# Performance work log

Measured on AMD Instinct MI355X. Metric: run time of the kernel, lower is better.

The kernel has to match this reference:

```python
import jax, jax.numpy as jnp
import numpy as np

B, N, C = 8, 4096, 512

def setup_inputs() -> dict:
    key = jax.random.key(0)
    ks = jax.random.split(key, 6)
    s = 1.0 / np.sqrt(C)
    return {
        "x": jax.random.normal(ks[0], (B, N, C), jnp.float32),
        "Wq": jax.random.normal(ks[1], (C, C), jnp.float32) * s,
        "Wk": jax.random.normal(ks[2], (C, C), jnp.float32) * s,
        "Wv": jax.random.normal(ks[3], (C, C), jnp.float32) * s,
        "W1": jax.random.normal(ks[4], (C, C), jnp.float32) * s,
        "W2": jax.random.normal(ks[5], (C, C), jnp.float32) * s,
    }

def reference(x, Wq, Wk, Wv, W1, W2):
    # torch nn.Linear: y = x @ W.T (bias=False)
    q = x @ Wq.T                      # [B,N,C]
    k = x @ Wk.T
    v = x @ Wv.T
    dim = q.shape[-1]
    q = jax.nn.softmax(q, axis=-1) * (dim ** -0.5)   # softmax over channels
    k = jax.nn.softmax(k, axis=-2)                   # softmax over sequence
    context = jnp.einsum('bnd,bne->bde', k, v)       # [B,C,C]
    attn = jnp.einsum('bnd,bde->bne', q, context)    # [B,N,C]
    x = attn + x
    return (x @ W1.T) @ W2.T + x
```

## Files before the change

kernel.cpp:

```cpp
#include <hip/hip_runtime.h>

typedef unsigned int uint;
typedef __bf16 bf16_t;
typedef bf16_t bf16x8 __attribute__((ext_vector_type(8)));
typedef float floatx4 __attribute__((ext_vector_type(4)));

struct __align__(8) us4 { unsigned short x, y, z, w; };

__device__ __forceinline__ unsigned short f2b(float f) {
    unsigned u = __float_as_uint(f);
    u = u + 0x7FFFu + ((u >> 16) & 1u);
    return (unsigned short)(u >> 16);
}
__device__ __forceinline__ float b2f(unsigned short h) {
    return __uint_as_float(((unsigned)h) << 16);
}

__device__ __forceinline__ void g2l16(const void* g, void* l) {
    __builtin_amdgcn_global_load_lds((__attribute__((address_space(1))) void*)g,
                                     (__attribute__((address_space(3))) void*)l,
                                     16, 0, 0);
}

template <int MODE, int NTN, bool BMS, int LD>
__global__ __launch_bounds__(512, 4) void gemm128(
    const unsigned short* __restrict__ A, const unsigned short* __restrict__ B,
    void* __restrict__ O, const unsigned short* __restrict__ R,
    unsigned short* __restrict__ O2, unsigned short* __restrict__ O3,
    float* __restrict__ Sq, float* __restrict__ Sk,
    const float* __restrict__ Sn,
    long long sB, float scale)
{
    __shared__ __attribute__((aligned(16))) unsigned short Ls[3][12288];

    const uint id = blockIdx.x;
    const int tid = threadIdx.x;
    const int l = tid & 63;
    const int w = tid >> 6;
    const int wm = (w >> 2) * 64;
    const int wnb = (w & 3) * 64;

    int arow0 = 0, n0 = 0, bb = 0;
    const unsigned short* Ab;
    const unsigned short* Bbp;
    long long pbase = 0;

    if constexpr (MODE == 6) {
        const uint xcd = id & 7;
        const uint g = id >> 3;
        const int t8 = (int)(g & 7);
        const int mt = t8 >> 1, ntc = t8 & 1;
        const int slice = (int)(g >> 3) * 8 + (int)xcd;
        const int b6 = slice >> 3, sk6 = slice & 7;
        Ab  = A + ((long long)b6 * 512 + mt  * 128) * 4096 + sk6 * 512;
        Bbp = B + ((long long)b6 * 512 + ntc * 256) * 4096 + sk6 * 512;
        pbase = (long long)slice * 262144 + (long long)mt * 128 * 512 + ntc * 256;
    } else {
        const uint xcd = id & 7;
        const uint g = id >> 3;
        const uint nt = g % NTN;
        const uint mg = g / NTN;
        const uint ms = mg * 8 + xcd;
        if constexpr (BMS) { bb = (int)(ms & 7); arow0 = bb * 4096 + (int)(ms >> 3) * 128; }
        else               { bb = 0;             arow0 = (int)ms * 128; }
        n0 = (int)nt * 256;
        Ab  = A + (long long)arow0 * LD;
        Bbp = B + (long long)bb * sB + (long long)n0 * LD;
    }

    const int q_ = tid >> 2;
    const int lc = (tid & 3) ^ ((tid >> 3) & 3);
    const unsigned short* pA  = Ab  + (long long)q_ * LD + lc * 8;
    const unsigned short* pB1 = Bbp + (long long)q_ * LD + lc * 8;
    const unsigned short* pB2 = Bbp + (long long)(128 + q_) * LD + lc * 8;

#define STG(bi, koff) do {                                                  \
        unsigned short* d_ = &Ls[bi][0] + tid * 8;                          \
        g2l16(pA  + (koff), d_);                                            \
        g2l16(pB1 + (koff), d_ + 4096);                                     \
        g2l16(pB2 + (koff), d_ + 8192);                                     \
    } while (0)

    const int fr = l & 15;
    const int c0 = l >> 4;
    const int swz = (c0 ^ ((fr >> 1) & 3)) << 4;
    const int aoff = (wm + fr) * 64 + swz;
    const int boff = (128 + wnb + fr) * 64 + swz;

    floatx4 acc[4][4] = {};

    STG(0, 0);
    STG(1, 32);
    asm volatile("s_waitcnt vmcnt(3)" ::: "memory");
    __builtin_amdgcn_s_barrier();

    int cur = 0, stb = 2;
    for (int t = 0; t < 16; ++t) {
        if (t + 2 < 16) STG(stb, (t + 2) * 32);

        const char* Lb = (const char*)&Ls[cur][0];
        bf16x8 af[4], bv[4];
#pragma unroll
        for (int i = 0; i < 4; ++i) af[i] = *(const bf16x8*)(Lb + aoff + i * 1024);
#pragma unroll
        for (int j = 0; j < 4; ++j) bv[j] = *(const bf16x8*)(Lb + boff + j * 1024);

        __builtin_amdgcn_s_setprio(1);
#pragma unroll
        for (int i = 0; i < 4; ++i)
#pragma unroll
            for (int j = 0; j < 4; ++j)
                acc[i][j] = __builtin_amdgcn_mfma_f32_16x16x32_bf16(
                    af[i], bv[j], acc[i][j], 0, 0, 0);
        __builtin_amdgcn_s_setprio(0);

        if (t < 15) {
            if (t < 14) asm volatile("s_waitcnt vmcnt(3)" ::: "memory");
            else        asm volatile("s_waitcnt vmcnt(0)" ::: "memory");
            __builtin_amdgcn_s_barrier();
        }
        cur = (cur == 2) ? 0 : cur + 1;
        stb = (stb == 2) ? 0 : stb + 1;
    }
#undef STG

    const int col = l & 15;
    const int rbase = (l >> 4) * 4;
    const int gm0 = arow0 + wm + rbase;
    const int gn0 = n0 + wnb + col;

    if constexpr (MODE == 6) {
        float* Pb = (float*)O + pbase;
#pragma unroll
        for (int i = 0; i < 4; ++i) {
            int lr = wm + i * 16 + rbase;
#pragma unroll
            for (int j = 0; j < 4; ++j) {
                int lcc = wnb + j * 16 + col;
#pragma unroll
                for (int r = 0; r < 4; ++r)
                    Pb[(long long)(lr + r) * 512 + lcc] = acc[i][j][r];
            }
        }
    } else if constexpr (MODE == 4) {
        if (n0 < 512) {
            unsigned short* Oq = (unsigned short*)O;
            float rs[4][4];
#pragma unroll
            for (int i = 0; i < 4; ++i)
#pragma unroll
                for (int r = 0; r < 4; ++r) rs[i][r] = 0.f;
#pragma unroll
            for (int i = 0; i < 4; ++i) {
                int gm = gm0 + i * 16;
#pragma unroll
                for (int j = 0; j < 4; ++j) {
                    int gn = gn0 + j * 16;
#pragma unroll
                    for (int r = 0; r < 4; ++r) {
                        float e = __expf(acc[i][j][r]);
                        rs[i][r] += e;
                        Oq[(long long)(gm + r) * 512 + gn] = f2b(e);
                    }
                }
            }
#pragma unroll
            for (int i = 0; i < 4; ++i)
#pragma unroll
                for (int r = 0; r < 4; ++r) {
                    float v = rs[i][r];
                    v += __shfl_xor(v, 1);
                    v += __shfl_xor(v, 2);
                    v += __shfl_xor(v, 4);
                    v += __shfl_xor(v, 8);
                    if ((l & 15) == 0)
                        atomicAdd(&Sq[gm0 + i * 16 + r], v);
                }
        } else if (n0 < 1024) {
            const int b = arow0 >> 12;
            const int mq0 = (arow0 & 4095) + wm + rbase;
            float cs[4] = {0.f, 0.f, 0.f, 0.f};
#pragma unroll
            for (int i = 0; i < 4; ++i) {
                int mq = mq0 + i * 16;
#pragma unroll
                for (int j = 0; j < 4; ++j) {
                    int d = gn0 + j * 16 - 512;
                    float e0 = __expf(acc[i][j][0]);
                    float e1 = __expf(acc[i][j][1]);
                    float e2 = __expf(acc[i][j][2]);
                    float e3 = __expf(acc[i][j][3]);
                    cs[j] += e0 + e1 + e2 + e3;
                    us4 pk = { f2b(e0), f2b(e1), f2b(e2), f2b(e3) };
                    *(us4*)(O2 + ((long long)b * 512 + d) * 4096 + mq) = pk;
                }
            }
#pragma unroll
            for (int j = 0; j < 4; ++j) {
                float v = cs[j];
                v += __shfl_xor(v, 16);
                v += __shfl_xor(v, 32);
                if (l < 16)
                    atomicAdd(&Sk[b * 512 + gn0 + j * 16 - 512], v);
            }
        } else {
            const int b = arow0 >> 12;
            const int mq0 = (arow0 & 4095) + wm + rbase;
#pragma unroll
            for (int i = 0; i < 4; ++i) {
                int mq = mq0 + i * 16;
#pragma unroll
                for (int j = 0; j < 4; ++j) {
                    int e_ = gn0 + j * 16 - 1024;
                    us4 pk = { f2b(acc[i][j][0]), f2b(acc[i][j][1]),
                               f2b(acc[i][j][2]), f2b(acc[i][j][3]) };
                    *(us4*)(O3 + ((long long)b * 512 + e_) * 4096 + mq) = pk;
                }
            }
        }
    } else if constexpr (MODE == 5) {
#pragma unroll
        for (int i = 0; i < 4; ++i) {
            int gm = gm0 + i * 16;
            float invs[4];
#pragma unroll
            for (int r = 0; r < 4; ++r) invs[r] = scale / Sn[gm + r];
#pragma unroll
            for (int j = 0; j < 4; ++j) {
                int gn = gn0 + j * 16;
#pragma unroll
                for (int r = 0; r < 4; ++r) {
                    long long idx = (long long)(gm + r) * 512 + gn;
                    ((unsigned short*)O)[idx] =
                        f2b(acc[i][j][r] * invs[r] + b2f(R[idx]));
                }
            }
        }
    } else {
#pragma unroll
        for (int i = 0; i < 4; ++i) {
            int gm = gm0 + i * 16;
#pragma unroll
            for (int j = 0; j < 4; ++j) {
                int gn = gn0 + j * 16;
#pragma unroll
                for (int r = 0; r < 4; ++r) {
                    long long idx = (long long)(gm + r) * 512 + gn;
                    float v = acc[i][j][r];
                    if constexpr (MODE == 0) {
                        ((unsigned short*)O)[idx] = f2b(v);
                    } else {
                        ((float*)O)[idx] = v + b2f(R[idx]);
                    }
                }
            }
        }
    }
}

__global__ __launch_bounds__(256) void wg_gemm(
    const unsigned short* __restrict__ W2b, const unsigned short* __restrict__ W1b,
    unsigned short* __restrict__ Wg)
{
    const int n = blockIdx.x;
    const int t = threadIdx.x;
    float a0 = 0.f, a1 = 0.f;
    const unsigned short* w2r = W2b + n * 512;
#pragma unroll 4
    for (int k = 0; k < 512; ++k) {
        float s = b2f(w2r[k]);
        a0 += s * b2f(W1b[k * 512 + t]);
        a1 += s * b2f(W1b[k * 512 + t + 256]);
    }
    Wg[n * 512 + t]       = f2b(a0);
    Wg[n * 512 + t + 256] = f2b(a1);
}

__global__ __launch_bounds__(256) void ctx_reduce(const float* __restrict__ P,
                                                  const float* __restrict__ Sk,
                                                  unsigned short* __restrict__ Ct)
{
    long long f = (long long)blockIdx.x * 256 + threadIdx.x;
    long long base = f * 4;
    int b = (int)(base >> 18);
    int rem = (int)(base & 262143);
    int d = rem & 511;
    float4 s = {0.f, 0.f, 0.f, 0.f};
#pragma unroll
    for (int sp = 0; sp < 8; ++sp) {
        float4 v = *(const float4*)(P + (long long)(b * 8 + sp) * 262144 + rem);
        s.x += v.x; s.y += v.y; s.z += v.z; s.w += v.w;
    }
    float4 sk = *(const float4*)(Sk + b * 512 + d);
    us4 o = { f2b(s.x / sk.x), f2b(s.y / sk.y), f2b(s.z / sk.z), f2b(s.w / sk.w) };
    *(us4*)(Ct + (long long)b * 262144 + rem) = o;
}

__global__ __launch_bounds__(256) void f32_to_bf16_k(const float* __restrict__ in,
                                                     unsigned short* __restrict__ out)
{
    long long i = ((long long)blockIdx.x * 256 + threadIdx.x) * 4;
    float4 v = *(const float4*)(in + i);
    us4 o = { f2b(v.x), f2b(v.y), f2b(v.z), f2b(v.w) };
    *(us4*)(out + i) = o;
}

struct WPtrs { const float* in[5]; unsigned short* out[5]; };
__global__ __launch_bounds__(256) void conv_weights(WPtrs p)
{
    int which = blockIdx.y;
    long long i = ((long long)blockIdx.x * 256 + threadIdx.x) * 4;
    float4 v = *(const float4*)(p.in[which] + i);
    us4 o = { f2b(v.x), f2b(v.y), f2b(v.z), f2b(v.w) };
    *(us4*)(p.out[which] + i) = o;
}

__global__ __launch_bounds__(256) void zero_f32(float* __restrict__ p)
{
    long long i = ((long long)blockIdx.x * 256 + threadIdx.x) * 4;
    *(float4*)(p + i) = make_float4(0.f, 0.f, 0.f, 0.f);
}

extern "C" void kernel_launch(void* const* d_in, const int* in_sizes, int n_in,
                              void* d_out, int out_size, void* d_ws, size_t ws_size,
                              hipStream_t stream)
{
    (void)in_sizes; (void)n_in; (void)out_size; (void)ws_size;
    const float* x  = (const float*)d_in[0];
    const float* Wq = (const float*)d_in[1];
    const float* Wk = (const float*)d_in[2];
    const float* Wv = (const float*)d_in[3];
    const float* W1 = (const float*)d_in[4];
    const float* W2 = (const float*)d_in[5];
    float* out = (float*)d_out;

    const int Bn = 8, N = 4096, C = 512;
    const long long M  = (long long)Bn * N;
    const long long XE = M * C;

    char* ws = (char*)d_ws;
    size_t off = 0;
    auto carve = [&](size_t bytes) -> void* {
        void* p = ws + off;
        off += (bytes + 255) & ~(size_t)255;
        return p;
    };

    unsigned short* xb   = (unsigned short*)carve(XE * 2);
    unsigned short* wcat = (unsigned short*)carve((size_t)3 * C * C * 2);
    unsigned short* w1b  = (unsigned short*)carve((size_t)C * C * 2);
    unsigned short* w2b  = (unsigned short*)carve((size_t)C * C * 2);
    unsigned short* wgb  = (unsigned short*)carve((size_t)C * C * 2);
    unsigned short* q    = (unsigned short*)carve(XE * 2);
    unsigned short* kT   = (unsigned short*)carve(XE * 2);
    unsigned short* vT   = (unsigned short*)carve(XE * 2);
    unsigned short* ctxT = (unsigned short*)carve((size_t)Bn * C * C * 2);
    float* Ssum = (float*)carve((size_t)(M + Bn * C) * 4);
    float* Sq = Ssum;
    float* Sk = Ssum + M;
    unsigned short* xr = kT;
    float* P = (float*)d_out;

    zero_f32<<<dim3(36), 256, 0, stream>>>(Ssum);

    f32_to_bf16_k<<<dim3((unsigned)(XE / 1024)), dim3(256), 0, stream>>>(x, xb);
    WPtrs wp = { { Wq, Wk, Wv, W1, W2 },
                 { wcat, wcat + C * C, wcat + 2 * C * C, w1b, w2b } };
    conv_weights<<<dim3((C * C) / 1024, 5), dim3(256), 0, stream>>>(wp);

    wg_gemm<<<dim3(512), 256, 0, stream>>>(w2b, w1b, wgb);

    gemm128<4, 6, false, 512><<<dim3(1536), 512, 0, stream>>>(
        xb, wcat, q, nullptr, kT, vT, Sq, Sk, nullptr, 0, 0.f);

    gemm128<6, 1, false, 4096><<<dim3(512), 512, 0, stream>>>(
        vT, kT, P, nullptr, nullptr, nullptr, nullptr, nullptr, nullptr,
        0, 0.f);
    ctx_reduce<<<dim3(2048), 256, 0, stream>>>(P, Sk, ctxT);

    gemm128<5, 2, true, 512><<<dim3(512), 512, 0, stream>>>(
        q, ctxT, xr, xb, nullptr, nullptr, nullptr, nullptr, Sq,
        (long long)C * C, 0.044194173824159216f);

    gemm128<3, 2, false, 512><<<dim3(512), 512, 0, stream>>>(
        xr, wgb, out, xr, nullptr, nullptr, nullptr, nullptr, nullptr,
        0, 0.f);
}
```

Measured before the change: 319.9 us.

## Reshape GEMM tiles to 256x128 with 4 waves and fuse prep kernels

Changes the GEMM block tile from 128x256 with 8 waves to 256x128 with 4 waves. Each wave now computes a 128x64 sub-tile with 8x4 MFMA accumulators, which raises per-wave register use and reuse of the B fragments. Grid mappings and NTN are adjusted so the launch counts stay the same. Separately, the zeroing, x conversion and Wq/Wk/Wv conversion kernels are merged into one prep kernel, and wg_gemm reads the fp32 W1/W2 directly and rounds them inline. Together these cut launches and an intermediate buffer, at the risk of lower occupancy from the larger accumulator set.

```diff
diff --git a/kernel.cpp b/kernel.cpp
--- a/kernel.cpp
+++ b/kernel.cpp
@@ -23,7 +23,7 @@
 }
 
 template <int MODE, int NTN, bool BMS, int LD>
-__global__ __launch_bounds__(512, 4) void gemm128(
+__global__ __launch_bounds__(256, 2) void gemm256x128(
     const unsigned short* __restrict__ A, const unsigned short* __restrict__ B,
     void* __restrict__ O, const unsigned short* __restrict__ R,
     unsigned short* __restrict__ O2, unsigned short* __restrict__ O3,
@@ -37,8 +37,8 @@
     const int tid = threadIdx.x;
     const int l = tid & 63;
     const int w = tid >> 6;
-    const int wm = (w >> 2) * 64;
-    const int wnb = (w & 3) * 64;
+    const int wm = (w >> 1) * 128;
+    const int wnb = (w & 1) * 64;
 
     int arow0 = 0, n0 = 0, bb = 0;
     const unsigned short* Ab;
@@ -49,49 +49,51 @@
         const uint xcd = id & 7;
         const uint g = id >> 3;
         const int t8 = (int)(g & 7);
-        const int mt = t8 >> 1, ntc = t8 & 1;
+        const int mt = t8 >> 2, ntc = t8 & 3;
         const int slice = (int)(g >> 3) * 8 + (int)xcd;
         const int b6 = slice >> 3, sk6 = slice & 7;
-        Ab  = A + ((long long)b6 * 512 + mt  * 128) * 4096 + sk6 * 512;
-        Bbp = B + ((long long)b6 * 512 + ntc * 256) * 4096 + sk6 * 512;
-        pbase = (long long)slice * 262144 + (long long)mt * 128 * 512 + ntc * 256;
+        Ab  = A + ((long long)b6 * 512 + mt  * 256) * 4096 + sk6 * 512;
+        Bbp = B + ((long long)b6 * 512 + ntc * 128) * 4096 + sk6 * 512;
+        pbase = (long long)slice * 262144 + (long long)mt * 256 * 512 + ntc * 128;
     } else {
         const uint xcd = id & 7;
         const uint g = id >> 3;
         const uint nt = g % NTN;
         const uint mg = g / NTN;
         const uint ms = mg * 8 + xcd;
-        if constexpr (BMS) { bb = (int)(ms & 7); arow0 = bb * 4096 + (int)(ms >> 3) * 128; }
-        else               { bb = 0;             arow0 = (int)ms * 128; }
-        n0 = (int)nt * 256;
+        if constexpr (BMS) { bb = (int)(ms & 7); arow0 = bb * 4096 + (int)(ms >> 3) * 256; }
+        else               { bb = 0;             arow0 = (int)ms * 256; }
+        n0 = (int)nt * 128;
         Ab  = A + (long long)arow0 * LD;
         Bbp = B + (long long)bb * sB + (long long)n0 * LD;
     }
 
     const int q_ = tid >> 2;
     const int lc = (tid & 3) ^ ((tid >> 3) & 3);
-    const unsigned short* pA  = Ab  + (long long)q_ * LD + lc * 8;
-    const unsigned short* pB1 = Bbp + (long long)q_ * LD + lc * 8;
-    const unsigned short* pB2 = Bbp + (long long)(128 + q_) * LD + lc * 8;
+    const unsigned short* pA = Ab  + (long long)q_ * LD + lc * 8;
+    const unsigned short* pB = Bbp + (long long)q_ * LD + lc * 8;
 
 #define STG(bi, koff) do {                                                  \
         unsigned short* d_ = &Ls[bi][0] + tid * 8;                          \
-        g2l16(pA  + (koff), d_);                                            \
-        g2l16(pB1 + (koff), d_ + 4096);                                     \
-        g2l16(pB2 + (koff), d_ + 8192);                                     \
+        g2l16(pA + (koff),                      d_);                        \
+        g2l16(pA + (long long) 64 * LD + (koff), d_ + 2048);                \
+        g2l16(pA + (long long)128 * LD + (koff), d_ + 4096);                \
+        g2l16(pA + (long long)192 * LD + (koff), d_ + 6144);                \
+        g2l16(pB + (koff),                      d_ + 8192);                 \
+        g2l16(pB + (long long) 64 * LD + (koff), d_ + 10240);               \
     } while (0)
 
     const int fr = l & 15;
     const int c0 = l >> 4;
     const int swz = (c0 ^ ((fr >> 1) & 3)) << 4;
     const int aoff = (wm + fr) * 64 + swz;
-    const int boff = (128 + wnb + fr) * 64 + swz;
-
-    floatx4 acc[4][4] = {};
+    const int boff = 16384 + (wnb + fr) * 64 + swz;
+
+    floatx4 acc[8][4] = {};
 
     STG(0, 0);
     STG(1, 32);
-    asm volatile("s_waitcnt vmcnt(3)" ::: "memory");
+    asm volatile("s_waitcnt vmcnt(6)" ::: "memory");
     __builtin_amdgcn_s_barrier();
 
     int cur = 0, stb = 2;
@@ -99,15 +101,15 @@
         if (t + 2 < 16) STG(stb, (t + 2) * 32);
 
         const char* Lb = (const char*)&Ls[cur][0];
-        bf16x8 af[4], bv[4];
-#pragma unroll
-        for (int i = 0; i < 4; ++i) af[i] = *(const bf16x8*)(Lb + aoff + i * 1024);
+        bf16x8 af[8], bv[4];
+#pragma unroll
+        for (int i = 0; i < 8; ++i) af[i] = *(const bf16x8*)(Lb + aoff + i * 1024);
 #pragma unroll
         for (int j = 0; j < 4; ++j) bv[j] = *(const bf16x8*)(Lb + boff + j * 1024);
 
         __builtin_amdgcn_s_setprio(1);
 #pragma unroll
-        for (int i = 0; i < 4; ++i)
+        for (int i = 0; i < 8; ++i)
 #pragma unroll
             for (int j = 0; j < 4; ++j)
                 acc[i][j] = __builtin_amdgcn_mfma_f32_16x16x32_bf16(
@@ -115,7 +117,7 @@
         __builtin_amdgcn_s_setprio(0);
 
         if (t < 15) {
-            if (t < 14) asm volatile("s_waitcnt vmcnt(3)" ::: "memory");
+            if (t < 14) asm volatile("s_waitcnt vmcnt(6)" ::: "memory");
             else        asm volatile("s_waitcnt vmcnt(0)" ::: "memory");
             __builtin_amdgcn_s_barrier();
         }
@@ -132,7 +134,7 @@
     if constexpr (MODE == 6) {
         float* Pb = (float*)O + pbase;
 #pragma unroll
-        for (int i = 0; i < 4; ++i) {
+        for (int i = 0; i < 8; ++i) {
             int lr = wm + i * 16 + rbase;
 #pragma unroll
             for (int j = 0; j < 4; ++j) {
@@ -145,13 +147,13 @@
     } else if constexpr (MODE == 4) {
         if (n0 < 512) {
             unsigned short* Oq = (unsigned short*)O;
-            float rs[4][4];
-#pragma unroll
-            for (int i = 0; i < 4; ++i)
+            float rs[8][4];
+#pragma unroll
+            for (int i = 0; i < 8; ++i)
 #pragma unroll
                 for (int r = 0; r < 4; ++r) rs[i][r] = 0.f;
 #pragma unroll
-            for (int i = 0; i < 4; ++i) {
+            for (int i = 0; i < 8; ++i) {
                 int gm = gm0 + i * 16;
 #pragma unroll
                 for (int j = 0; j < 4; ++j) {
@@ -165,7 +167,7 @@
                 }
             }
 #pragma unroll
-            for (int i = 0; i < 4; ++i)
+            for (int i = 0; i < 8; ++i)
 #pragma unroll
                 for (int r = 0; r < 4; ++r) {
                     float v = rs[i][r];
@@ -181,7 +183,7 @@
             const int mq0 = (arow0 & 4095) + wm + rbase;
             float cs[4] = {0.f, 0.f, 0.f, 0.f};
 #pragma unroll
-            for (int i = 0; i < 4; ++i) {
+            for (int i = 0; i < 8; ++i) {
                 int mq = mq0 + i * 16;
 #pragma unroll
                 for (int j = 0; j < 4; ++j) {
@@ -207,7 +209,7 @@
             const int b = arow0 >> 12;
             const int mq0 = (arow0 & 4095) + wm + rbase;
 #pragma unroll
-            for (int i = 0; i < 4; ++i) {
+            for (int i = 0; i < 8; ++i) {
                 int mq = mq0 + i * 16;
 #pragma unroll
                 for (int j = 0; j < 4; ++j) {
@@ -220,7 +222,7 @@
         }
     } else if constexpr (MODE == 5) {
 #pragma unroll
-        for (int i = 0; i < 4; ++i) {
+        for (int i = 0; i < 8; ++i) {
             int gm = gm0 + i * 16;
             float invs[4];
 #pragma unroll
@@ -238,7 +240,7 @@
         }
     } else {
 #pragma unroll
-        for (int i = 0; i < 4; ++i) {
+        for (int i = 0; i < 8; ++i) {
             int gm = gm0 + i * 16;
 #pragma unroll
             for (int j = 0; j < 4; ++j) {
@@ -259,18 +261,18 @@
 }
 
 __global__ __launch_bounds__(256) void wg_gemm(
-    const unsigned short* __restrict__ W2b, const unsigned short* __restrict__ W1b,
+    const float* __restrict__ W2, const float* __restrict__ W1,
     unsigned short* __restrict__ Wg)
 {
     const int n = blockIdx.x;
     const int t = threadIdx.x;
     float a0 = 0.f, a1 = 0.f;
-    const unsigned short* w2r = W2b + n * 512;
-#pragma unroll 4
+    const float* w2r = W2 + n * 512;
+#pragma unroll 8
     for (int k = 0; k < 512; ++k) {
-        float s = b2f(w2r[k]);
-        a0 += s * b2f(W1b[k * 512 + t]);
-        a1 += s * b2f(W1b[k * 512 + t + 256]);
+        float s = b2f(f2b(w2r[k]));
+        a0 += s * b2f(f2b(W1[k * 512 + t]));
+        a1 += s * b2f(f2b(W1[k * 512 + t + 256]));
     }
     Wg[n * 512 + t]       = f2b(a0);
     Wg[n * 512 + t + 256] = f2b(a1);
@@ -296,29 +298,31 @@
     *(us4*)(Ct + (long long)b * 262144 + rem) = o;
 }
 
-__global__ __launch_bounds__(256) void f32_to_bf16_k(const float* __restrict__ in,
-                                                     unsigned short* __restrict__ out)
-{
-    long long i = ((long long)blockIdx.x * 256 + threadIdx.x) * 4;
-    float4 v = *(const float4*)(in + i);
-    us4 o = { f2b(v.x), f2b(v.y), f2b(v.z), f2b(v.w) };
-    *(us4*)(out + i) = o;
-}
-
-struct WPtrs { const float* in[5]; unsigned short* out[5]; };
-__global__ __launch_bounds__(256) void conv_weights(WPtrs p)
-{
-    int which = blockIdx.y;
-    long long i = ((long long)blockIdx.x * 256 + threadIdx.x) * 4;
-    float4 v = *(const float4*)(p.in[which] + i);
-    us4 o = { f2b(v.x), f2b(v.y), f2b(v.z), f2b(v.w) };
-    *(us4*)(p.out[which] + i) = o;
-}
-
-__global__ __launch_bounds__(256) void zero_f32(float* __restrict__ p)
-{
-    long long i = ((long long)blockIdx.x * 256 + threadIdx.x) * 4;
-    *(float4*)(p + i) = make_float4(0.f, 0.f, 0.f, 0.f);
+__global__ __launch_bounds__(256) void prep(
+    const float* __restrict__ x, unsigned short* __restrict__ xb,
+    const float* __restrict__ Wq, const float* __restrict__ Wk,
+    const float* __restrict__ Wv, unsigned short* __restrict__ wcat,
+    float* __restrict__ Ssum)
+{
+    const int bid = blockIdx.x;
+    const int t = threadIdx.x;
+    if (bid < 16384) {
+        long long i = ((long long)bid * 256 + t) * 4;
+        float4 v = *(const float4*)(x + i);
+        us4 o = { f2b(v.x), f2b(v.y), f2b(v.z), f2b(v.w) };
+        *(us4*)(xb + i) = o;
+    } else if (bid < 17152) {
+        int wb = bid - 16384;
+        int which = wb >> 8;
+        const float* src = which == 0 ? Wq : (which == 1 ? Wk : Wv);
+        long long i = ((long long)(wb & 255) * 256 + t) * 4;
+        float4 v = *(const float4*)(src + i);
+        us4 o = { f2b(v.x), f2b(v.y), f2b(v.z), f2b(v.w) };
+        *(us4*)(wcat + (long long)which * 262144 + i) = o;
+    } else {
+        long long i = ((long long)(bid - 17152) * 256 + t) * 4;
+        *(float4*)(Ssum + i) = make_float4(0.f, 0.f, 0.f, 0.f);
+    }
 }
 
 extern "C" void kernel_launch(void* const* d_in, const int* in_sizes, int n_in,
@@ -348,8 +352,6 @@
 
     unsigned short* xb   = (unsigned short*)carve(XE * 2);
     unsigned short* wcat = (unsigned short*)carve((size_t)3 * C * C * 2);
-    unsigned short* w1b  = (unsigned short*)carve((size_t)C * C * 2);
-    unsigned short* w2b  = (unsigned short*)carve((size_t)C * C * 2);
     unsigned short* wgb  = (unsigned short*)carve((size_t)C * C * 2);
     unsigned short* q    = (unsigned short*)carve(XE * 2);
     unsigned short* kT   = (unsigned short*)carve(XE * 2);
@@ -361,28 +363,23 @@
     unsigned short* xr = kT;
     float* P = (float*)d_out;
 
-    zero_f32<<<dim3(36), 256, 0, stream>>>(Ssum);
-
-    f32_to_bf16_k<<<dim3((unsigned)(XE / 1024)), dim3(256), 0, stream>>>(x, xb);
-    WPtrs wp = { { Wq, Wk, Wv, W1, W2 },
-                 { wcat, wcat + C * C, wcat + 2 * C * C, w1b, w2b } };
-    conv_weights<<<dim3((C * C) / 1024, 5), dim3(256), 0, stream>>>(wp);
-
-    wg_gemm<<<dim3(512), 256, 0, stream>>>(w2b, w1b, wgb);
-
-    gemm128<4, 6, false, 512><<<dim3(1536), 512, 0, stream>>>(
+    prep<<<dim3(17188), 256, 0, stream>>>(x, xb, Wq, Wk, Wv, wcat, Ssum);
+
+    wg_gemm<<<dim3(512), 256, 0, stream>>>(W2, W1, wgb);
+
+    gemm256x128<4, 12, false, 512><<<dim3(1536), 256, 0, stream>>>(
         xb, wcat, q, nullptr, kT, vT, Sq, Sk, nullptr, 0, 0.f);
 
-    gemm128<6, 1, false, 4096><<<dim3(512), 512, 0, stream>>>(
+    gemm256x128<6, 1, false, 4096><<<dim3(512), 256, 0, stream>>>(
         vT, kT, P, nullptr, nullptr, nullptr, nullptr, nullptr, nullptr,
         0, 0.f);
     ctx_reduce<<<dim3(2048), 256, 0, stream>>>(P, Sk, ctxT);
 
-    gemm128<5, 2, true, 512><<<dim3(512), 512, 0, stream>>>(
+    gemm256x128<5, 4, true, 512><<<dim3(512), 256, 0, stream>>>(
         q, ctxT, xr, xb, nullptr, nullptr, nullptr, nullptr, Sq,
         (long long)C * C, 0.044194173824159216f);
 
-    gemm128<3, 2, false, 512><<<dim3(512), 512, 0, stream>>>(
+    gemm256x128<3, 4, false, 512><<<dim3(512), 256, 0, stream>>>(
         xr, wgb, out, xr, nullptr, nullptr, nullptr, nullptr, nullptr,
         0, 0.f);
 }
```

Result: no change. 321.7 us (+0.6%).
